# Performance work log

Measured on AMD Instinct MI355X. Metric: run time of the kernel, lower is better.

## Reference

```python
import jax, jax.numpy as jnp
import numpy as np

N_NODES = 50000
N_EDGES = 320000
HIDDEN = 256
EDGE_DIM = 64
NUM_HEADS = 8
HEAD_DIM = HIDDEN // NUM_HEADS


def setup_inputs() -> dict:
    key = jax.random.key(0)
    ks = jax.random.split(key, 9)
    s = HIDDEN ** -0.5
    return {
        "x": jax.random.normal(ks[0], (N_NODES, HIDDEN), dtype=jnp.float32),
        "edge_index": jax.random.randint(ks[1], (2, N_EDGES), 0, N_NODES, dtype=jnp.int64),
        "edge_attr": jax.random.normal(ks[2], (N_EDGES, EDGE_DIM), dtype=jnp.float32),
        "Wq": jax.random.normal(ks[3], (HIDDEN, HIDDEN), dtype=jnp.float32) * s,
        "Wk": jax.random.normal(ks[4], (HIDDEN, HIDDEN), dtype=jnp.float32) * s,
        "Wv": jax.random.normal(ks[5], (HIDDEN, HIDDEN), dtype=jnp.float32) * s,
        "We": jax.random.normal(ks[6], (EDGE_DIM, NUM_HEADS), dtype=jnp.float32) * (EDGE_DIM ** -0.5),
        "Wo": jax.random.normal(ks[7], (HIDDEN, HIDDEN), dtype=jnp.float32) * s,
        "bo": jnp.zeros((HIDDEN,), dtype=jnp.float32),
    }


def reference(x, edge_index, edge_attr, Wq, Wk, Wv, We, Wo, bo):
    N = x.shape[0]
    # node projections -> (N, H, Dh)
    Q = (x @ Wq).reshape(N, NUM_HEADS, HEAD_DIM)
    K = (x @ Wk).reshape(N, NUM_HEADS, HEAD_DIM)
    V = (x @ Wv).reshape(N, NUM_HEADS, HEAD_DIM)
    src, tgt = edge_index[0], edge_index[1]
    Q_src = Q[src]   # (E, H, Dh)
    K_tgt = K[tgt]
    V_tgt = V[tgt]
    scale = jnp.float32(HEAD_DIM ** -0.5)
    # per-edge, per-head scores with edge bias: (E, H)
    score = (Q_src * K_tgt).sum(axis=-1) * scale + edge_attr @ We
    # segment softmax over tgt (all heads at once)
    m = jax.ops.segment_max(score, tgt, num_segments=N)          # (N, H)
    ex = jnp.exp(score - m[tgt])                                  # (E, H)
    den = jax.ops.segment_sum(ex, tgt, num_segments=N)           # (N, H)
    attn = ex / den[tgt]                                          # (E, H)
    # weighted scatter-add of V per head -> (N, H, Dh)
    agg = jax.ops.segment_sum(attn[:, :, None] * V_tgt, tgt, num_segments=N)
    out = agg.reshape(N, HIDDEN) @ Wo + bo
    return out
```

## Files before the change

### kernel.cpp

```cpp
#include <hip/hip_runtime.h>
#include <hip/hip_bf16.h>

#define NN 50000
#define NE 320000
#define HID 256
#define NBLK_FLAG 1250
#define FLAG_MAGIC 0x7F3A9C51

typedef __attribute__((ext_vector_type(8))) short bf16x8;
typedef __attribute__((ext_vector_type(4))) float f32x4;

static __device__ __forceinline__ short f2bf(float f) {
    union { __hip_bfloat16 h; short s; } u;
    u.h = __float2bfloat16(f);
    return u.s;
}

__global__ void prep_k(const int* __restrict__ ei, int* __restrict__ flags,
                       const float* __restrict__ Wv, const float* __restrict__ Wo,
                       unsigned short* __restrict__ wsB) {
    const int b = blockIdx.x;
    if (b < NBLK_FLAG) {
        __shared__ int nz;
        if (threadIdx.x == 0) nz = 0;
        __syncthreads();
        unsigned hv = ((const unsigned*)ei)[2 * threadIdx.x + 1];
        if (hv != 0u) nz = 1;
        __syncthreads();
        const int is64 = (nz == 0);
        const int e = b * 256 + threadIdx.x;
        if (e < NE) {
            int t = is64 ? ei[2 * (NE + e)] : ei[NE + e];
            if (t >= 0 && t < NN) flags[t] = FLAG_MAGIC;
        }
    } else {
        const int i = b - NBLK_FLAG;
        const int j = threadIdx.x;
        const float* wv = Wv + i * HID;
        float s0 = 0.f, s1 = 0.f, s2 = 0.f, s3 = 0.f;
        #pragma unroll 8
        for (int k = 0; k < HID; k += 4) {
            s0 = fmaf(wv[k + 0], Wo[(k + 0) * HID + j], s0);
            s1 = fmaf(wv[k + 1], Wo[(k + 1) * HID + j], s1);
            s2 = fmaf(wv[k + 2], Wo[(k + 2) * HID + j], s2);
            s3 = fmaf(wv[k + 3], Wo[(k + 3) * HID + j], s3);
        }
        const float acc = (s0 + s1) + (s2 + s3);
        const int kt = i >> 6, kp = i & 63;
        const int kk = kp >> 5, h = (kp >> 3) & 3, e = kp & 7;
        wsB[(kt * 32768 + (j >> 4) * 2048 + kk * 1024 + h * 256 + (j & 15) * 16 + e * 2) >> 1]
            = (unsigned short)f2bf(acc);
    }
}


#define CS_STRIDE 260

__global__ __launch_bounds__(256, 4) void out_gemm_k(
    const float* __restrict__ x, const unsigned short* __restrict__ wsB,
    const float* __restrict__ bo, const int* __restrict__ flags,
    float* __restrict__ out)
{
    __shared__ char lds[32768];
    float* Cs = (float*)lds;

    const int tid  = threadIdx.x;
    const int wave = tid >> 6;
    const int lane = tid & 63;
    const int rl   = lane & 15;
    const int hi   = lane >> 4;
    const int row0 = blockIdx.x * 32;
    const int wcol = wave * 64;

    #pragma unroll
    for (int i = 0; i < 8; ++i) {
        const int r = wave * 8 + i;
        int grow = row0 + r; if (grow >= NN) grow = NN - 1;
        const float* src = x + (size_t)grow * HID + ((lane ^ (r & 7)) << 2);
        __builtin_amdgcn_global_load_lds(
            (const __attribute__((address_space(1))) unsigned int*)src,
            (__attribute__((address_space(3))) unsigned int*)(lds + r * 1024),
            16, 0, 0);
    }

    const char* gB = (const char*)wsB + wave * 8192 + lane * 16;
    bf16x8 bA[4][2], bB[4][2];
    #pragma unroll
    for (int n = 0; n < 4; ++n)
        #pragma unroll
        for (int kk = 0; kk < 2; ++kk)
            bA[n][kk] = *(const bf16x8*)(gB + n * 2048 + kk * 1024);
    float bov[4];
    #pragma unroll
    for (int n = 0; n < 4; ++n) bov[n] = bo[wcol + n * 16 + rl];

    __syncthreads();

    f32x4 acc[2][4];
    #pragma unroll
    for (int m = 0; m < 2; ++m)
        #pragma unroll
        for (int n = 0; n < 4; ++n)
            acc[m][n] = (f32x4){0.f, 0.f, 0.f, 0.f};

    int4 flg[2];

    auto step = [&](const int kt, bf16x8 (&bcur)[4][2], bf16x8 (&bnext)[4][2], const bool pf) {
        if (pf) {
            #pragma unroll
            for (int n = 0; n < 4; ++n)
                #pragma unroll
                for (int kk = 0; kk < 2; ++kk)
                    bnext[n][kk] = *(const bf16x8*)(gB + (kt + 1) * 32768 + n * 2048 + kk * 1024);
        }
        #pragma unroll
        for (int kk = 0; kk < 2; ++kk) {
            bf16x8 af[2];
            #pragma unroll
            for (int m = 0; m < 2; ++m) {
                const int r = m * 16 + rl;
                const int j0 = kt * 16 + kk * 8 + hi * 2;
                const int s = r & 7;
                const f32x4 lo = *(const f32x4*)(lds + r * 1024 + ((j0 ^ s) << 4));
                const f32x4 h4 = *(const f32x4*)(lds + r * 1024 + (((j0 + 1) ^ s) << 4));
                bf16x8 w;
                w[0] = f2bf(lo[0]); w[1] = f2bf(lo[1]); w[2] = f2bf(lo[2]); w[3] = f2bf(lo[3]);
                w[4] = f2bf(h4[0]); w[5] = f2bf(h4[1]); w[6] = f2bf(h4[2]); w[7] = f2bf(h4[3]);
                af[m] = w;
            }
            #pragma unroll
            for (int m = 0; m < 2; ++m)
                #pragma unroll
                for (int n = 0; n < 4; ++n)
                    acc[m][n] = __builtin_amdgcn_mfma_f32_16x16x32_bf16(af[m], bcur[n][kk], acc[m][n], 0, 0, 0);
        }
    };
    step(0, bA, bB, true);
    step(1, bB, bA, true);
    #pragma unroll
    for (int m = 0; m < 2; ++m)
        flg[m] = *(const int4*)(flags + row0 + m * 16 + hi * 4);
    step(2, bA, bB, true);
    step(3, bB, bA, false);

    #pragma unroll
    for (int h2 = 0; h2 < 2; ++h2) {
        __syncthreads();
        const int fl[4] = {flg[h2].x, flg[h2].y, flg[h2].z, flg[h2].w};
        #pragma unroll
        for (int j = 0; j < 4; ++j) {
            const float msk = (fl[j] == FLAG_MAGIC) ? 1.f : 0.f;
            float* crow = Cs + (hi * 4 + j) * CS_STRIDE + wcol + rl;
            #pragma unroll
            for (int n = 0; n < 4; ++n)
                crow[n * 16] = fmaf(msk, acc[h2][n][j], bov[n]);
        }
        __syncthreads();
        #pragma unroll
        for (int i = 0; i < 4; ++i) {
            const int rloc = wave * 4 + i;
            const f32x4 v = *(const f32x4*)(Cs + rloc * CS_STRIDE + lane * 4);
            const int r = row0 + h2 * 16 + rloc;
            if (r < NN)
                *(f32x4*)(out + (size_t)r * HID + lane * 4) = v;
        }
    }
}


extern "C" void kernel_launch(void* const* d_in, const int* in_sizes, int n_in,
                              void* d_out, int out_size, void* d_ws, size_t ws_size,
                              hipStream_t stream) {
    const float* x   = (const float*)d_in[0];
    const int*   ei  = (const int*)d_in[1];
    const float* Wv  = (const float*)d_in[5];
    const float* Wo  = (const float*)d_in[7];
    const float* bo  = (const float*)d_in[8];
    float* out = (float*)d_out;

    unsigned short* wsB = (unsigned short*)d_ws;
    int* flags = (int*)((char*)d_ws + 4 * 32768);

    prep_k<<<NBLK_FLAG + HID, 256, 0, stream>>>(ei, flags, Wv, Wo, wsB);

    dim3 grid((NN + 31) / 32);
    out_gemm_k<<<grid, 256, 0, stream>>>(x, wsB, bo, flags, out);
}
```

Measured before the change: 36.10 us.

## Pre-convert x to bf16 fragment layout in a prep kernel

Adds a conversion stage to the first kernel that reads x once and writes it as bf16 in the exact MFMA fragment order. The GEMM kernel then loads A fragments straight from global memory into registers, double-buffered across k-steps, with no LDS staging or in-loop fp32→bf16 conversion. LDS use shrinks to the output-staging buffer and one barrier is dropped. The cost is an extra pass that writes and re-reads a bf16 copy of x, which raises total memory traffic unless the copy stays in the last-level cache.

```diff
diff --git a/kernel.cpp b/kernel.cpp
--- a/kernel.cpp
+++ b/kernel.cpp
@@ -4,8 +4,14 @@
 #define NN 50000
 #define NE 320000
 #define HID 256
+#define NT 1563
+#define NBLK_CVT NT
 #define NBLK_FLAG 1250
 #define FLAG_MAGIC 0x7F3A9C51
+
+#define XB_BYTES (NT * 16384)
+#define WSB_OFF  XB_BYTES
+#define FLAGS_OFF (XB_BYTES + 131072)
 
 typedef __attribute__((ext_vector_type(8))) short bf16x8;
 typedef __attribute__((ext_vector_type(4))) float f32x4;
@@ -16,26 +22,46 @@
     return u.s;
 }
 
-__global__ void prep_k(const int* __restrict__ ei, int* __restrict__ flags,
-                       const float* __restrict__ Wv, const float* __restrict__ Wo,
-                       unsigned short* __restrict__ wsB) {
+__global__ void stage1_k(const float* __restrict__ x, const int* __restrict__ ei,
+                         const float* __restrict__ Wv, const float* __restrict__ Wo,
+                         char* __restrict__ xb, unsigned short* __restrict__ wsB,
+                         int* __restrict__ flags) {
     const int b = blockIdx.x;
-    if (b < NBLK_FLAG) {
+    const int tid = threadIdx.x;
+    if (b < NBLK_CVT) {
+        const int t = b;
+        const int l = tid & 63;
+        const int rl = l & 15, g = l >> 4;
+        #pragma unroll
+        for (int i = 0; i < 4; ++i) {
+            const int f = (tid >> 6) + 4 * i;
+            const int kt = f >> 2, m = (f >> 1) & 1, kk = f & 1;
+            int row = t * 32 + m * 16 + rl;
+            if (row >= NN) row = NN - 1;
+            const float* src = x + (size_t)row * HID + kt * 64 + kk * 32 + g * 8;
+            const f32x4 lo = __builtin_nontemporal_load((const f32x4*)src);
+            const f32x4 h4 = __builtin_nontemporal_load((const f32x4*)(src + 4));
+            bf16x8 w;
+            w[0] = f2bf(lo[0]); w[1] = f2bf(lo[1]); w[2] = f2bf(lo[2]); w[3] = f2bf(lo[3]);
+            w[4] = f2bf(h4[0]); w[5] = f2bf(h4[1]); w[6] = f2bf(h4[2]); w[7] = f2bf(h4[3]);
+            *(bf16x8*)(xb + (size_t)t * 16384 + f * 1024 + l * 16) = w;
+        }
+    } else if (b < NBLK_CVT + NBLK_FLAG) {
         __shared__ int nz;
-        if (threadIdx.x == 0) nz = 0;
+        if (tid == 0) nz = 0;
         __syncthreads();
-        unsigned hv = ((const unsigned*)ei)[2 * threadIdx.x + 1];
+        unsigned hv = ((const unsigned*)ei)[2 * tid + 1];
         if (hv != 0u) nz = 1;
         __syncthreads();
         const int is64 = (nz == 0);
-        const int e = b * 256 + threadIdx.x;
+        const int e = (b - NBLK_CVT) * 256 + tid;
         if (e < NE) {
-            int t = is64 ? ei[2 * (NE + e)] : ei[NE + e];
-            if (t >= 0 && t < NN) flags[t] = FLAG_MAGIC;
+            int tg = is64 ? ei[2 * (NE + e)] : ei[NE + e];
+            if (tg >= 0 && tg < NN) flags[tg] = FLAG_MAGIC;
         }
     } else {
-        const int i = b - NBLK_FLAG;
-        const int j = threadIdx.x;
+        const int i = b - NBLK_CVT - NBLK_FLAG;
+        const int j = tid;
         const float* wv = Wv + i * HID;
         float s0 = 0.f, s1 = 0.f, s2 = 0.f, s3 = 0.f;
         #pragma unroll 8
@@ -57,11 +83,11 @@
 #define CS_STRIDE 260
 
 __global__ __launch_bounds__(256, 4) void out_gemm_k(
-    const float* __restrict__ x, const unsigned short* __restrict__ wsB,
+    const char* __restrict__ xb, const unsigned short* __restrict__ wsB,
     const float* __restrict__ bo, const int* __restrict__ flags,
     float* __restrict__ out)
 {
-    __shared__ char lds[32768];
+    __shared__ char lds[16640];
     float* Cs = (float*)lds;
 
     const int tid  = threadIdx.x;
@@ -72,30 +98,35 @@
     const int row0 = blockIdx.x * 32;
     const int wcol = wave * 64;
 
-    #pragma unroll
-    for (int i = 0; i < 8; ++i) {
-        const int r = wave * 8 + i;
-        int grow = row0 + r; if (grow >= NN) grow = NN - 1;
-        const float* src = x + (size_t)grow * HID + ((lane ^ (r & 7)) << 2);
-        __builtin_amdgcn_global_load_lds(
-            (const __attribute__((address_space(1))) unsigned int*)src,
-            (__attribute__((address_space(3))) unsigned int*)(lds + r * 1024),
-            16, 0, 0);
-    }
+    const char* gA = xb + (size_t)blockIdx.x * 16384 + lane * 16;
+    const char* gB = (const char*)wsB + wave * 8192 + lane * 16;
 
-    const char* gB = (const char*)wsB + wave * 8192 + lane * 16;
-    bf16x8 bA[4][2], bB[4][2];
-    #pragma unroll
-    for (int n = 0; n < 4; ++n)
-        #pragma unroll
-        for (int kk = 0; kk < 2; ++kk)
-            bA[n][kk] = *(const bf16x8*)(gB + n * 2048 + kk * 1024);
-    float bov[4];
-    #pragma unroll
-    for (int n = 0; n < 4; ++n) bov[n] = bo[wcol + n * 16 + rl];
+#define LOAD_A(DST, KT) do {                                               \
+        _Pragma("unroll")                                                  \
+        for (int q_ = 0; q_ < 4; ++q_)                     \
+            DST[q_] = *(const bf16x8*)(gA + ((KT) * 4 + q_) * 1024);       \
+    } while (0)
 
-    __syncthreads();
+#define LOAD_B(KT) do {                                                    \
+        _Pragma("unroll")                                                  \
+        for (int n_ = 0; n_ < 4; ++n_) {                                   \
+            bfrag[n_][0] = *(const bf16x8*)(gB + (KT) * 32768 + n_ * 2048);\
+            bfrag[n_][1] = *(const bf16x8*)(gB + (KT) * 32768 + n_ * 2048 + 1024); \
+        }                                                                  \
+    } while (0)
 
+#define MFMA_KT(A) do {                                                    \
+        _Pragma("unroll")                                                  \
+        for (int kk_ = 0; kk_ < 2; ++kk_)                                  \
+            _Pragma("unroll")                                              \
+            for (int m_ = 0; m_ < 2; ++m_)                                 \
+                _Pragma("unroll")                                          \
+                for (int n_ = 0; n_ < 4; ++n_)                             \
+                    acc[m_][n_] = __builtin_amdgcn_mfma_f32_16x16x32_bf16( \
+                        A[m_ * 2 + kk_], bfrag[n_][kk_], acc[m_][n_], 0, 0, 0); \
+    } while (0)
+
+    bf16x8 aA[4], aB[4], bfrag[4][2];
     f32x4 acc[2][4];
     #pragma unroll
     for (int m = 0; m < 2; ++m)
@@ -103,49 +134,29 @@
         for (int n = 0; n < 4; ++n)
             acc[m][n] = (f32x4){0.f, 0.f, 0.f, 0.f};
 
+    LOAD_A(aA, 0);
+    LOAD_B(0);
+    float bov[4];
+    #pragma unroll
+    for (int n = 0; n < 4; ++n) bov[n] = bo[wcol + n * 16 + rl];
+
     int4 flg[2];
 
-    auto step = [&](const int kt, bf16x8 (&bcur)[4][2], bf16x8 (&bnext)[4][2], const bool pf) {
-        if (pf) {
-            #pragma unroll
-            for (int n = 0; n < 4; ++n)
-                #pragma unroll
-                for (int kk = 0; kk < 2; ++kk)
-                    bnext[n][kk] = *(const bf16x8*)(gB + (kt + 1) * 32768 + n * 2048 + kk * 1024);
-        }
-        #pragma unroll
-        for (int kk = 0; kk < 2; ++kk) {
-            bf16x8 af[2];
-            #pragma unroll
-            for (int m = 0; m < 2; ++m) {
-                const int r = m * 16 + rl;
-                const int j0 = kt * 16 + kk * 8 + hi * 2;
-                const int s = r & 7;
-                const f32x4 lo = *(const f32x4*)(lds + r * 1024 + ((j0 ^ s) << 4));
-                const f32x4 h4 = *(const f32x4*)(lds + r * 1024 + (((j0 + 1) ^ s) << 4));
-                bf16x8 w;
-                w[0] = f2bf(lo[0]); w[1] = f2bf(lo[1]); w[2] = f2bf(lo[2]); w[3] = f2bf(lo[3]);
-                w[4] = f2bf(h4[0]); w[5] = f2bf(h4[1]); w[6] = f2bf(h4[2]); w[7] = f2bf(h4[3]);
-                af[m] = w;
-            }
-            #pragma unroll
-            for (int m = 0; m < 2; ++m)
-                #pragma unroll
-                for (int n = 0; n < 4; ++n)
-                    acc[m][n] = __builtin_amdgcn_mfma_f32_16x16x32_bf16(af[m], bcur[n][kk], acc[m][n], 0, 0, 0);
-        }
-    };
-    step(0, bA, bB, true);
-    step(1, bB, bA, true);
+    LOAD_A(aB, 1);  MFMA_KT(aA);  LOAD_B(1);
+    LOAD_A(aA, 2);  MFMA_KT(aB);  LOAD_B(2);
+    LOAD_A(aB, 3);  MFMA_KT(aA);  LOAD_B(3);
     #pragma unroll
     for (int m = 0; m < 2; ++m)
         flg[m] = *(const int4*)(flags + row0 + m * 16 + hi * 4);
-    step(2, bA, bB, true);
-    step(3, bB, bA, false);
+    MFMA_KT(aB);
+
+#undef LOAD_A
+#undef LOAD_B
+#undef MFMA_KT
 
     #pragma unroll
     for (int h2 = 0; h2 < 2; ++h2) {
-        __syncthreads();
+        if (h2) __syncthreads();
         const int fl[4] = {flg[h2].x, flg[h2].y, flg[h2].z, flg[h2].w};
         #pragma unroll
         for (int j = 0; j < 4; ++j) {
@@ -178,11 +189,10 @@
     const float* bo  = (const float*)d_in[8];
     float* out = (float*)d_out;
 
-    unsigned short* wsB = (unsigned short*)d_ws;
-    int* flags = (int*)((char*)d_ws + 4 * 32768);
+    char* xb = (char*)d_ws;
+    unsigned short* wsB = (unsigned short*)((char*)d_ws + WSB_OFF);
+    int* flags = (int*)((char*)d_ws + FLAGS_OFF);
 
-    prep_k<<<NBLK_FLAG + HID, 256, 0, stream>>>(ei, flags, Wv, Wo, wsB);
-
-    dim3 grid((NN + 31) / 32);
-    out_gemm_k<<<grid, 256, 0, stream>>>(x, wsB, bo, flags, out);
+    stage1_k<<<NBLK_CVT + NBLK_FLAG + HID, 256, 0, stream>>>(x, ei, Wv, Wo, xb, wsB, flags);
+    out_gemm_k<<<NT, 256, 0, stream>>>(xb, wsB, bo, flags, out);
 }
```

New measurement: 44.89 us. 1.24x slower.
